# Performance work log

Measured on AMD Instinct MI355X. Metric: run time of the kernel, lower is better.

The kernel has to match this reference:

```python
import jax, jax.numpy as jnp
import numpy as np


def _cmul(x, y):
    # complex multiply with real/imag stacked in last dim of size 2
    xr, xi = x[..., 0], x[..., 1]
    yr, yi = y[..., 0], y[..., 1]
    return jnp.stack([xr * yr - xi * yi, xr * yi + xi * yr], axis=-1)


def setup_inputs() -> dict:
    key = jax.random.key(0)
    k1, k2, k3 = jax.random.split(key, 3)
    B, N, H, W = 2, 64, 512, 512
    f_ipt = jax.random.normal(k1, (B, H, W, 2), dtype=jnp.float32)
    f_y = jax.random.normal(k2, (B, N, H, W, 2), dtype=jnp.float32)
    Hreal = jax.random.normal(k3, (N, H, W, 2), dtype=jnp.float32)
    return {"f_ipt": f_ipt, "f_y": f_y, "Hreal": Hreal, "NBFkeep": N}


def reference(f_ipt, f_y, Hreal, NBFkeep):
    # fmult: z_f = Hreal_f * ph (ab is expanded but unused in the original; f_ab is zeros)
    # broadcast: Hreal [N,H,W,2], f_ipt [B,H,W,2] -> z [B,N,H,W,2]
    z = _cmul(Hreal[None], f_ipt[:, None])
    diff = z - f_y
    # ftran('Ph'): conj(Hreal) * diff, summed over frame axis, / NBFkeep
    conjH = jnp.stack([Hreal[..., 0], -Hreal[..., 1]], axis=-1)
    g = jnp.sum(_cmul(conjH[None], diff), axis=1) / NBFkeep  # [B,H,W,2]
    return g
```

## Files before the change

kernel.cpp:

```cpp
#include <hip/hip_runtime.h>
#include <hip/hip_bf16.h>


__global__ void __launch_bounds__(256) idt_fused_kernel(
    const float4* __restrict__ H4,
    const float4* __restrict__ Y4,
    const float4* __restrict__ X4,
    float4* __restrict__ O4,
    const int* __restrict__ nbf,
    int N, int P)
{
    int p = blockIdx.x * blockDim.x + threadIdx.x;
    if (p >= P) return;

    float s0 = 0.f, s1 = 0.f;
    float a00r = 0.f, a00i = 0.f, a01r = 0.f, a01i = 0.f;
    float a10r = 0.f, a10i = 0.f, a11r = 0.f, a11i = 0.f;

    const float4* hp = H4 + p;
    const float4* y0 = Y4 + p;
    const float4* y1 = Y4 + (size_t)N * P + p;

    #pragma unroll 4
    for (int n = 0; n < N; ++n) {
        float4 hv = hp[(size_t)n * P];
        float4 v0 = y0[(size_t)n * P];
        float4 v1 = y1[(size_t)n * P];

        s0 += hv.x * hv.x + hv.y * hv.y;
        s1 += hv.z * hv.z + hv.w * hv.w;

        a00r += hv.x * v0.x + hv.y * v0.y;
        a00i += hv.x * v0.y - hv.y * v0.x;
        a01r += hv.z * v0.z + hv.w * v0.w;
        a01i += hv.z * v0.w - hv.w * v0.z;

        a10r += hv.x * v1.x + hv.y * v1.y;
        a10i += hv.x * v1.y - hv.y * v1.x;
        a11r += hv.z * v1.z + hv.w * v1.w;
        a11i += hv.z * v1.w - hv.w * v1.z;
    }

    float inv = 1.0f / (float)nbf[0];

    float4 x0 = X4[p];
    float4 x1 = X4[(size_t)P + p];

    float4 o0, o1;
    o0.x = (x0.x * s0 - a00r) * inv;
    o0.y = (x0.y * s0 - a00i) * inv;
    o0.z = (x0.z * s1 - a01r) * inv;
    o0.w = (x0.w * s1 - a01i) * inv;

    o1.x = (x1.x * s0 - a10r) * inv;
    o1.y = (x1.y * s0 - a10i) * inv;
    o1.z = (x1.z * s1 - a11r) * inv;
    o1.w = (x1.w * s1 - a11i) * inv;

    O4[p] = o0;
    O4[(size_t)P + p] = o1;
}

extern "C" void kernel_launch(void* const* d_in, const int* in_sizes, int n_in,
                              void* d_out, int out_size, void* d_ws, size_t ws_size,
                              hipStream_t stream) {
    const float* f_ipt = (const float*)d_in[0];
    const float* f_y   = (const float*)d_in[1];
    const float* Hreal = (const float*)d_in[2];
    const int*   nbf   = (const int*)d_in[3];

    const int B = in_sizes[1] / in_sizes[2];
    const int N = in_sizes[1] / in_sizes[0];
    const int P = in_sizes[0] / B / 4;

    dim3 block(256);
    dim3 grid((P + block.x - 1) / block.x);
    idt_fused_kernel<<<grid, block, 0, stream>>>(
        (const float4*)Hreal, (const float4*)f_y, (const float4*)f_ipt,
        (float4*)d_out, nbf, N, P);
}
```

Measured before the change: 432.7 us.

## Split frame reduction across grid y-dimension and combine with atomics

Each thread's serial loop over the N frames is split into SPLIT=4 segments, each handled by a separate block row in the y-dimension. Partial results are combined with float atomicAdd into an output zeroed by hipMemsetAsync. This quadruples the block count so more loads are in flight on a kernel that otherwise launches only a few blocks per CU. The cost is an extra memset, eight atomics per thread, and a summation order that is no longer deterministic.

```diff
diff --git a/kernel.cpp b/kernel.cpp
--- a/kernel.cpp
+++ b/kernel.cpp
@@ -2,30 +2,35 @@
 #include <hip/hip_bf16.h>
 
 
-__global__ void __launch_bounds__(256) idt_fused_kernel(
+constexpr int SPLIT = 4;
+
+__global__ void __launch_bounds__(256) idt_partial_kernel(
     const float4* __restrict__ H4,
     const float4* __restrict__ Y4,
     const float4* __restrict__ X4,
-    float4* __restrict__ O4,
+    float* __restrict__ O,
     const int* __restrict__ nbf,
-    int N, int P)
+    int N, int P, int nseg)
 {
     int p = blockIdx.x * blockDim.x + threadIdx.x;
     if (p >= P) return;
+
+    int n0 = blockIdx.y * nseg;
+    int n1 = min(N, n0 + nseg);
 
     float s0 = 0.f, s1 = 0.f;
     float a00r = 0.f, a00i = 0.f, a01r = 0.f, a01i = 0.f;
     float a10r = 0.f, a10i = 0.f, a11r = 0.f, a11i = 0.f;
 
-    const float4* hp = H4 + p;
-    const float4* y0 = Y4 + p;
-    const float4* y1 = Y4 + (size_t)N * P + p;
+    const float4* hp = H4 + (size_t)n0 * P + p;
+    const float4* y0 = Y4 + (size_t)n0 * P + p;
+    const float4* y1 = Y4 + ((size_t)N + n0) * P + p;
 
     #pragma unroll 4
-    for (int n = 0; n < N; ++n) {
-        float4 hv = hp[(size_t)n * P];
-        float4 v0 = y0[(size_t)n * P];
-        float4 v1 = y1[(size_t)n * P];
+    for (int n = n0; n < n1; ++n) {
+        float4 hv = *hp; hp += P;
+        float4 v0 = *y0; y0 += P;
+        float4 v1 = *y1; y1 += P;
 
         s0 += hv.x * hv.x + hv.y * hv.y;
         s1 += hv.z * hv.z + hv.w * hv.w;
@@ -46,19 +51,18 @@
     float4 x0 = X4[p];
     float4 x1 = X4[(size_t)P + p];
 
-    float4 o0, o1;
-    o0.x = (x0.x * s0 - a00r) * inv;
-    o0.y = (x0.y * s0 - a00i) * inv;
-    o0.z = (x0.z * s1 - a01r) * inv;
-    o0.w = (x0.w * s1 - a01i) * inv;
+    float* ob0 = O + (size_t)p * 4;
+    float* ob1 = O + ((size_t)P + p) * 4;
 
-    o1.x = (x1.x * s0 - a10r) * inv;
-    o1.y = (x1.y * s0 - a10i) * inv;
-    o1.z = (x1.z * s1 - a11r) * inv;
-    o1.w = (x1.w * s1 - a11i) * inv;
+    atomicAdd(ob0 + 0, (x0.x * s0 - a00r) * inv);
+    atomicAdd(ob0 + 1, (x0.y * s0 - a00i) * inv);
+    atomicAdd(ob0 + 2, (x0.z * s1 - a01r) * inv);
+    atomicAdd(ob0 + 3, (x0.w * s1 - a01i) * inv);
 
-    O4[p] = o0;
-    O4[(size_t)P + p] = o1;
+    atomicAdd(ob1 + 0, (x1.x * s0 - a10r) * inv);
+    atomicAdd(ob1 + 1, (x1.y * s0 - a10i) * inv);
+    atomicAdd(ob1 + 2, (x1.z * s1 - a11r) * inv);
+    atomicAdd(ob1 + 3, (x1.w * s1 - a11i) * inv);
 }
 
 extern "C" void kernel_launch(void* const* d_in, const int* in_sizes, int n_in,
@@ -72,10 +76,13 @@
     const int B = in_sizes[1] / in_sizes[2];
     const int N = in_sizes[1] / in_sizes[0];
     const int P = in_sizes[0] / B / 4;
+    const int nseg = (N + SPLIT - 1) / SPLIT;
+
+    hipMemsetAsync(d_out, 0, (size_t)out_size * sizeof(float), stream);
 
     dim3 block(256);
-    dim3 grid((P + block.x - 1) / block.x);
-    idt_fused_kernel<<<grid, block, 0, stream>>>(
+    dim3 grid((P + block.x - 1) / block.x, SPLIT);
+    idt_partial_kernel<<<grid, block, 0, stream>>>(
         (const float4*)Hreal, (const float4*)f_y, (const float4*)f_ipt,
-        (float4*)d_out, nbf, N, P);
+        (float*)d_out, nbf, N, P, nseg);
 }
```

Measured after the change: 464.5 us. 1.07x slower.

## Split frame reduction across four thread rows with shared-memory combine

Applied to the files above, without the earlier changes.

Each block now has 256x4 threads. The frame axis is split into four segments, each thread accumulates partial sums over its segment, and the partials are combined through shared memory before one row writes the output. This gives four times more threads and more outstanding loads per pixel, to better hide memory latency in a bandwidth-bound kernel. In exchange it adds shared memory use, a barrier and lower per-block occupancy, and it assumes N is divisible by 4.

```diff
diff --git a/kernel.cpp b/kernel.cpp
--- a/kernel.cpp
+++ b/kernel.cpp
@@ -2,63 +2,83 @@
 #include <hip/hip_bf16.h>
 
 
-__global__ void __launch_bounds__(256) idt_fused_kernel(
-    const float4* __restrict__ H4,
-    const float4* __restrict__ Y4,
-    const float4* __restrict__ X4,
-    float4* __restrict__ O4,
+typedef float f4 __attribute__((ext_vector_type(4)));
+
+__global__ void __launch_bounds__(1024) idt_fused_kernel(
+    const f4* __restrict__ H4,
+    const f4* __restrict__ Y4,
+    const f4* __restrict__ X4,
+    f4* __restrict__ O4,
     const int* __restrict__ nbf,
     int N, int P)
 {
-    int p = blockIdx.x * blockDim.x + threadIdx.x;
-    if (p >= P) return;
+    __shared__ float red[4][256][10];
 
-    float s0 = 0.f, s1 = 0.f;
-    float a00r = 0.f, a00i = 0.f, a01r = 0.f, a01i = 0.f;
-    float a10r = 0.f, a10i = 0.f, a11r = 0.f, a11i = 0.f;
+    const int tx = threadIdx.x;
+    const int ty = threadIdx.y;
+    const int p  = blockIdx.x * 256 + tx;
 
-    const float4* hp = H4 + p;
-    const float4* y0 = Y4 + p;
-    const float4* y1 = Y4 + (size_t)N * P + p;
+    const int nseg = N >> 2;
+    const int n0   = ty * nseg;
 
-    #pragma unroll 4
-    for (int n = 0; n < N; ++n) {
-        float4 hv = hp[(size_t)n * P];
-        float4 v0 = y0[(size_t)n * P];
-        float4 v1 = y1[(size_t)n * P];
+    float acc[10];
+    #pragma unroll
+    for (int j = 0; j < 10; ++j) acc[j] = 0.f;
 
-        s0 += hv.x * hv.x + hv.y * hv.y;
-        s1 += hv.z * hv.z + hv.w * hv.w;
+    if (p < P) {
+        const f4* hp = H4 + (size_t)n0 * P + p;
+        const f4* y0 = Y4 + (size_t)n0 * P + p;
+        const f4* y1 = Y4 + ((size_t)N + n0) * P + p;
 
-        a00r += hv.x * v0.x + hv.y * v0.y;
-        a00i += hv.x * v0.y - hv.y * v0.x;
-        a01r += hv.z * v0.z + hv.w * v0.w;
-        a01i += hv.z * v0.w - hv.w * v0.z;
+        #pragma unroll 4
+        for (int n = 0; n < nseg; ++n) {
+            f4 hv = *hp; hp += P;
+            f4 v0 = *y0; y0 += P;
+            f4 v1 = *y1; y1 += P;
 
-        a10r += hv.x * v1.x + hv.y * v1.y;
-        a10i += hv.x * v1.y - hv.y * v1.x;
-        a11r += hv.z * v1.z + hv.w * v1.w;
-        a11i += hv.z * v1.w - hv.w * v1.z;
+            acc[0] += hv.x * hv.x + hv.y * hv.y;
+            acc[1] += hv.z * hv.z + hv.w * hv.w;
+
+            acc[2] += hv.x * v0.x + hv.y * v0.y;
+            acc[3] += hv.x * v0.y - hv.y * v0.x;
+            acc[4] += hv.z * v0.z + hv.w * v0.w;
+            acc[5] += hv.z * v0.w - hv.w * v0.z;
+
+            acc[6] += hv.x * v1.x + hv.y * v1.y;
+            acc[7] += hv.x * v1.y - hv.y * v1.x;
+            acc[8] += hv.z * v1.z + hv.w * v1.w;
+            acc[9] += hv.z * v1.w - hv.w * v1.z;
+        }
     }
 
-    float inv = 1.0f / (float)nbf[0];
+    #pragma unroll
+    for (int j = 0; j < 10; ++j) red[ty][tx][j] = acc[j];
+    __syncthreads();
 
-    float4 x0 = X4[p];
-    float4 x1 = X4[(size_t)P + p];
+    if (ty == 0 && p < P) {
+        float r[10];
+        #pragma unroll
+        for (int j = 0; j < 10; ++j)
+            r[j] = red[0][tx][j] + red[1][tx][j] + red[2][tx][j] + red[3][tx][j];
 
-    float4 o0, o1;
-    o0.x = (x0.x * s0 - a00r) * inv;
-    o0.y = (x0.y * s0 - a00i) * inv;
-    o0.z = (x0.z * s1 - a01r) * inv;
-    o0.w = (x0.w * s1 - a01i) * inv;
+        const float inv = 1.0f / (float)nbf[0];
+        f4 x0 = X4[p];
+        f4 x1 = X4[(size_t)P + p];
 
-    o1.x = (x1.x * s0 - a10r) * inv;
-    o1.y = (x1.y * s0 - a10i) * inv;
-    o1.z = (x1.z * s1 - a11r) * inv;
-    o1.w = (x1.w * s1 - a11i) * inv;
+        f4 o0, o1;
+        o0.x = (x0.x * r[0] - r[2]) * inv;
+        o0.y = (x0.y * r[0] - r[3]) * inv;
+        o0.z = (x0.z * r[1] - r[4]) * inv;
+        o0.w = (x0.w * r[1] - r[5]) * inv;
 
-    O4[p] = o0;
-    O4[(size_t)P + p] = o1;
+        o1.x = (x1.x * r[0] - r[6]) * inv;
+        o1.y = (x1.y * r[0] - r[7]) * inv;
+        o1.z = (x1.z * r[1] - r[8]) * inv;
+        o1.w = (x1.w * r[1] - r[9]) * inv;
+
+        O4[p] = o0;
+        O4[(size_t)P + p] = o1;
+    }
 }
 
 extern "C" void kernel_launch(void* const* d_in, const int* in_sizes, int n_in,
@@ -73,9 +93,9 @@
     const int N = in_sizes[1] / in_sizes[0];
     const int P = in_sizes[0] / B / 4;
 
-    dim3 block(256);
-    dim3 grid((P + block.x - 1) / block.x);
+    dim3 block(256, 4);
+    dim3 grid((P + 255) / 256);
     idt_fused_kernel<<<grid, block, 0, stream>>>(
-        (const float4*)Hreal, (const float4*)f_y, (const float4*)f_ipt,
-        (float4*)d_out, nbf, N, P);
+        (const f4*)Hreal, (const f4*)f_y, (const f4*)f_ipt,
+        (f4*)d_out, nbf, N, P);
 }
```

Measured after the change: 437.1 us. No clear change (+1.0%).
